# Performance work log

Hardware: AMD Instinct MI355X
Metric: run time of the kernel (lower is better)

The kernel has to match this reference:

```python
import jax, jax.numpy as jnp
import numpy as np


def setup_inputs() -> dict:
    key = jax.random.key(0)
    kx, kt = jax.random.split(key)
    b, n, d = 4, 4096, 1024
    x = jax.random.normal(kx, (b, n, d), dtype=jnp.float32)
    t = jax.random.normal(kt, (n, d), dtype=jnp.float32)
    return {"x": x, "t": t}


def reference(x, t):
    # y[b,i,d] = sum_{j<=i} t[i-j,d] * x[b,j,d]
    # Causal depthwise Toeplitz matvec == linear convolution truncated to n.
    # Computed via FFT along the sequence axis (zero-pad to 2n so the
    # circular convolution equals the linear one on the first n outputs).
    b, n, d = x.shape
    L = 2 * n
    xf = jnp.fft.rfft(x.astype(jnp.float32), n=L, axis=1)        # (b, L/2+1, d) complex
    tf = jnp.fft.rfft(t.astype(jnp.float32), n=L, axis=0)        # (L/2+1, d) complex
    y = jnp.fft.irfft(xf * tf[None], n=L, axis=1)[:, :n, :]      # (b, n, d)
    return y.astype(x.dtype)
```

## Files before the change

### kernel.cpp

```cpp
#include <hip/hip_runtime.h>

#define NT 512
#define SCL (1.0f / 8192.0f)
#define PI_F 3.14159265358979323846f

__device__ __forceinline__ int P(int i) { return i ^ ((i >> 5) & 31); }

__device__ __forceinline__ float2 cmul(float2 a, float2 b) {
  return make_float2(a.x * b.x - a.y * b.y, a.x * b.y + a.y * b.x);
}
__device__ __forceinline__ float2 csqr(float2 a) {
  return make_float2(a.x * a.x - a.y * a.y, 2.f * a.x * a.y);
}
__device__ __forceinline__ float2 cadd(float2 a, float2 b) { return make_float2(a.x + b.x, a.y + b.y); }
__device__ __forceinline__ float2 csub(float2 a, float2 b) { return make_float2(a.x - b.x, a.y - b.y); }
__device__ __forceinline__ float2 cmuli (float2 a) { return make_float2(-a.y,  a.x); }
__device__ __forceinline__ float2 cmulmi(float2 a) { return make_float2( a.y, -a.x); }

constexpr float RT2 = 0.70710678118654752440f;
constexpr float CQ1 = 0.92387953251128675613f;
constexpr float SQ1 = 0.38268343236508977173f;
constexpr float C8x[4] = {1.f,  RT2, 0.f, -RT2};
constexpr float C8y[4] = {0.f, -RT2, -1.f, -RT2};

template<bool UNIT>
__device__ __forceinline__ void r8_fwd(float2* e, float2 b) {
  float2 b2, b4;
  if (!UNIT) { b2 = csqr(b); b4 = csqr(b2); }
  #pragma unroll
  for (int j = 0; j < 4; ++j) {
    float2 u = e[j], v = e[j + 4];
    float2 d = csub(u, v);
    e[j] = cadd(u, v);
    float2 c8 = make_float2(C8x[j], C8y[j]);
    if (UNIT) e[j + 4] = (j == 0) ? d : cmul(d, c8);
    else      e[j + 4] = cmul(d, (j == 0) ? b : cmul(b, c8));
  }
  #pragma unroll
  for (int o = 0; o < 8; o += 4) {
    #pragma unroll
    for (int j = 0; j < 2; ++j) {
      float2 u = e[o + j], v = e[o + j + 2];
      float2 d = csub(u, v);
      e[o + j] = cadd(u, v);
      if (UNIT) e[o + j + 2] = (j == 0) ? d : cmulmi(d);
      else      e[o + j + 2] = cmul(d, (j == 0) ? b2 : cmulmi(b2));
    }
  }
  #pragma unroll
  for (int o = 0; o < 8; o += 2) {
    float2 u = e[o], v = e[o + 1];
    float2 d = csub(u, v);
    e[o] = cadd(u, v);
    e[o + 1] = UNIT ? d : cmul(d, b4);
  }
}

template<bool UNIT>
__device__ __forceinline__ void r8_inv(float2* e, float2 g) {
  float2 g2, g4;
  if (!UNIT) { g2 = csqr(g); g4 = csqr(g2); }
  #pragma unroll
  for (int o = 0; o < 8; o += 2) {
    float2 t = UNIT ? e[o + 1] : cmul(e[o + 1], g4);
    float2 u = e[o];
    e[o] = cadd(u, t); e[o + 1] = csub(u, t);
  }
  #pragma unroll
  for (int o = 0; o < 8; o += 4) {
    #pragma unroll
    for (int j = 0; j < 2; ++j) {
      float2 v = e[o + j + 2];
      float2 t;
      if (UNIT) t = (j == 0) ? v : cmuli(v);
      else      t = cmul(v, (j == 0) ? g2 : cmuli(g2));
      float2 u = e[o + j];
      e[o + j] = cadd(u, t); e[o + j + 2] = csub(u, t);
    }
  }
  #pragma unroll
  for (int j = 0; j < 4; ++j) {
    float2 v = e[j + 4];
    float2 t;
    float2 c8c = make_float2(C8x[j], -C8y[j]);
    if (UNIT) t = (j == 0) ? v : cmul(v, c8c);
    else      t = cmul(v, (j == 0) ? g : cmul(g, c8c));
    float2 u = e[j];
    e[j] = cadd(u, t); e[j + 4] = csub(u, t);
  }
}

__device__ __forceinline__ void trip8_fwd(float2* cb, int base, int G, float2 b) {
  #pragma unroll 1
  for (int g = 0; g < 2; ++g) {
    int bs = base + g * 4096;
    float2 e[8];
    #pragma unroll
    for (int j = 0; j < 8; ++j) e[j] = cb[P(bs + G * j)];
    r8_fwd<false>(e, b);
    #pragma unroll
    for (int j = 0; j < 8; ++j) cb[P(bs + G * j)] = e[j];
  }
}

__device__ __forceinline__ void trip8_inv(float2* cb, int base, int G, float2 g) {
  #pragma unroll 1
  for (int gg = 0; gg < 2; ++gg) {
    int bs = base + gg * 4096;
    float2 e[8];
    #pragma unroll
    for (int j = 0; j < 8; ++j) e[j] = cb[P(bs + G * j)];
    r8_inv<false>(e, g);
    #pragma unroll
    for (int j = 0; j < 8; ++j) cb[P(bs + G * j)] = e[j];
  }
}

__global__ __launch_bounds__(NT)
void fftconv(float* __restrict__ xT, const float* __restrict__ tT) {
  __shared__ float2 cb[8192];
  __shared__ float2 Th[8192];
  const int tid = threadIdx.x;
  const int d = blockIdx.x;

  const int baseA = tid;
  const int baseB = ((tid >> 6) << 9) + (tid & 63);
  const int baseC = ((tid >> 3) << 6) + (tid & 7);
  const int baseM = tid << 3;

  float s0, c0; __sincosf(-PI_F * (float)tid / 2048.f, &s0, &c0);
  const float2 bA = make_float2(c0, s0);
  float s1, c1; __sincosf(-PI_F * (float)(tid & 63) / 256.f, &s1, &c1);
  const float2 bB = make_float2(c1, s1);
  float s2, c2; __sincosf(-PI_F * (float)(tid & 7) / 32.f, &s2, &c2);
  const float2 bC = make_float2(c2, s2);
  float sw, cw; __sincosf(-PI_F * (float)tid / 4096.f, &sw, &cw);
  const float2 W0 = make_float2(cw, sw);
  const float2 ROT  = make_float2(CQ1, -SQ1);
  const float2 ROTc = make_float2(CQ1,  SQ1);

  {
    const float* tp = tT + (size_t)d * 4096;
    float2 w = W0;
    #pragma unroll
    for (int k = 0; k < 8; ++k) {
      int n = tid + NT * k;
      float tv = tp[n];
      cb[P(n)] = make_float2(tv, 0.f);
      cb[P(n + 4096)] = make_float2(tv * w.x, tv * w.y);
      w = cmul(w, ROT);
    }
  }
  __syncthreads();
  trip8_fwd(cb, baseA, 512, bA); __syncthreads();
  trip8_fwd(cb, baseB, 64,  bB); __syncthreads();
  trip8_fwd(cb, baseC, 8,   bC); __syncthreads();
  #pragma unroll 1
  for (int g = 0; g < 2; ++g) {
    int bs = baseM + g * 4096;
    float2 e[8];
    #pragma unroll
    for (int j = 0; j < 8; ++j) e[j] = cb[P(bs + j)];
    r8_fwd<true>(e, make_float2(1.f, 0.f));
    #pragma unroll
    for (int j = 0; j < 8; ++j) Th[P(bs + j)] = make_float2(e[j].x * SCL, e[j].y * SCL);
  }
  __syncthreads();

  #pragma unroll 1
  for (int pass = 0; pass < 2; ++pass) {
    float* r0 = xT + ((size_t)(2 * pass)     * 1024 + d) * 4096;
    float* r1 = xT + ((size_t)(2 * pass + 1) * 1024 + d) * 4096;
    {
      float2 w = W0;
      #pragma unroll
      for (int k = 0; k < 8; ++k) {
        int n = tid + NT * k;
        float2 v = make_float2(r0[n], r1[n]);
        cb[P(n)] = v;
        cb[P(n + 4096)] = cmul(v, w);
        w = cmul(w, ROT);
      }
    }
    __syncthreads();
    trip8_fwd(cb, baseA, 512, bA); __syncthreads();
    trip8_fwd(cb, baseB, 64,  bB); __syncthreads();
    trip8_fwd(cb, baseC, 8,   bC); __syncthreads();
    #pragma unroll 1
    for (int g = 0; g < 2; ++g) {
      int bs = baseM + g * 4096;
      float2 e[8];
      #pragma unroll
      for (int j = 0; j < 8; ++j) e[j] = cb[P(bs + j)];
      r8_fwd<true>(e, make_float2(1.f, 0.f));
      #pragma unroll
      for (int j = 0; j < 8; ++j) e[j] = cmul(e[j], Th[P(bs + j)]);
      r8_inv<true>(e, make_float2(1.f, 0.f));
      #pragma unroll
      for (int j = 0; j < 8; ++j) cb[P(bs + j)] = e[j];
    }
    __syncthreads();
    trip8_inv(cb, baseC, 8,   make_float2(bC.x, -bC.y)); __syncthreads();
    trip8_inv(cb, baseB, 64,  make_float2(bB.x, -bB.y)); __syncthreads();
    trip8_inv(cb, baseA, 512, make_float2(bA.x, -bA.y)); __syncthreads();
    {
      float2 w = make_float2(cw, -sw);
      #pragma unroll
      for (int k = 0; k < 8; ++k) {
        int n = tid + NT * k;
        float2 u = cb[P(n)];
        float2 v = cmul(cb[P(n + 4096)], w);
        r0[n] = u.x + v.x;
        r1[n] = u.y + v.y;
        w = cmul(w, ROTc);
      }
    }
    __syncthreads();
  }
}

__global__ __launch_bounds__(256)
void transpose64(const float* __restrict__ src, float* __restrict__ dst, int R, int C) {
  __shared__ float tile[64][65];
  int t  = threadIdx.x;
  int c4 = t & 15;
  int r  = t >> 4;
  size_t slab = (size_t)blockIdx.z * (size_t)R * (size_t)C;
  const float* s = src + slab;
  float* dd = dst + slab;
  int col0 = blockIdx.x * 64, row0 = blockIdx.y * 64;
  #pragma unroll
  for (int k = 0; k < 4; ++k) {
    int rr = r + 16 * k;
    const float4 v = *(const float4*)(s + (size_t)(row0 + rr) * C + col0 + 4 * c4);
    tile[rr][4 * c4 + 0] = v.x;
    tile[rr][4 * c4 + 1] = v.y;
    tile[rr][4 * c4 + 2] = v.z;
    tile[rr][4 * c4 + 3] = v.w;
  }
  __syncthreads();
  #pragma unroll
  for (int k = 0; k < 4; ++k) {
    int cc = r + 16 * k;
    float4 w;
    w.x = tile[4 * c4 + 0][cc];
    w.y = tile[4 * c4 + 1][cc];
    w.z = tile[4 * c4 + 2][cc];
    w.w = tile[4 * c4 + 3][cc];
    *(float4*)(dd + (size_t)(col0 + cc) * R + row0 + 4 * c4) = w;
  }
}

extern "C" void kernel_launch(void* const* d_in, const int* in_sizes, int n_in,
                              void* d_out, int out_size, void* d_ws, size_t ws_size,
                              hipStream_t stream) {
  const float* x = (const float*)d_in[0];
  const float* t = (const float*)d_in[1];
  float* out = (float*)d_out;
  float* ws  = (float*)d_ws;
  float* xT  = ws;
  float* tT  = ws + (size_t)4 * 1024 * 4096;

  transpose64<<<dim3(16, 64, 4), 256, 0, stream>>>(x, xT, 4096, 1024);
  transpose64<<<dim3(16, 64, 1), 256, 0, stream>>>(t, tT, 4096, 1024);

  fftconv<<<dim3(1024), NT, 0, stream>>>(xT, tT);

  transpose64<<<dim3(64, 16, 4), 256, 0, stream>>>(xT, out, 1024, 4096);
}
```

Measured before the change: 183.3 us.

## Precompute filter spectrum in separate kernel to halve fftconv shared memory

Moves the FFT of the Toeplitz filter t into its own kernel that writes the scaled spectrum to global memory, using the output buffer as scratch. The main fftconv kernel then loads the spectrum from global memory in the pointwise-multiply stage and keeps only one 64 KB shared buffer instead of two. The intent is to allow more blocks per CU and better latency hiding. The cost is an extra launch plus a write and reread of the spectrum through global memory, and the spectrum is now read once per pass rather than computed once per block.

```diff
diff --git a/kernel.cpp b/kernel.cpp
--- a/kernel.cpp
+++ b/kernel.cpp
@@ -117,9 +117,59 @@
 }
 
 __global__ __launch_bounds__(NT)
-void fftconv(float* __restrict__ xT, const float* __restrict__ tT) {
+void that8(const float* __restrict__ tT, float2* __restrict__ ThG) {
   __shared__ float2 cb[8192];
-  __shared__ float2 Th[8192];
+  const int tid = threadIdx.x;
+  const int d = blockIdx.x;
+
+  const int baseA = tid;
+  const int baseB = ((tid >> 6) << 9) + (tid & 63);
+  const int baseC = ((tid >> 3) << 6) + (tid & 7);
+  const int baseM = tid << 3;
+
+  float s0, c0; __sincosf(-PI_F * (float)tid / 2048.f, &s0, &c0);
+  const float2 bA = make_float2(c0, s0);
+  float s1, c1; __sincosf(-PI_F * (float)(tid & 63) / 256.f, &s1, &c1);
+  const float2 bB = make_float2(c1, s1);
+  float s2, c2; __sincosf(-PI_F * (float)(tid & 7) / 32.f, &s2, &c2);
+  const float2 bC = make_float2(c2, s2);
+  float sw, cw; __sincosf(-PI_F * (float)tid / 4096.f, &sw, &cw);
+  const float2 W0 = make_float2(cw, sw);
+  const float2 ROT = make_float2(CQ1, -SQ1);
+
+  {
+    const float* tp = tT + (size_t)d * 4096;
+    float2 w = W0;
+    #pragma unroll
+    for (int k = 0; k < 8; ++k) {
+      int n = tid + NT * k;
+      float tv = tp[n];
+      cb[P(n)] = make_float2(tv, 0.f);
+      cb[P(n + 4096)] = make_float2(tv * w.x, tv * w.y);
+      w = cmul(w, ROT);
+    }
+  }
+  __syncthreads();
+  trip8_fwd(cb, baseA, 512, bA); __syncthreads();
+  trip8_fwd(cb, baseB, 64,  bB); __syncthreads();
+  trip8_fwd(cb, baseC, 8,   bC); __syncthreads();
+  float2* thg = ThG + (size_t)d * 8192;
+  #pragma unroll 1
+  for (int g = 0; g < 2; ++g) {
+    int bs = baseM + g * 4096;
+    float2 e[8];
+    #pragma unroll
+    for (int j = 0; j < 8; ++j) e[j] = cb[P(bs + j)];
+    r8_fwd<true>(e, make_float2(1.f, 0.f));
+    #pragma unroll
+    for (int j = 0; j < 8; ++j)
+      thg[tid + 512 * j + 4096 * g] = make_float2(e[j].x * SCL, e[j].y * SCL);
+  }
+}
+
+__global__ __launch_bounds__(NT)
+void fftconv(float* __restrict__ xT, const float2* __restrict__ ThG) {
+  __shared__ float2 cb[8192];
   const int tid = threadIdx.x;
   const int d = blockIdx.x;
 
@@ -139,33 +189,7 @@
   const float2 ROT  = make_float2(CQ1, -SQ1);
   const float2 ROTc = make_float2(CQ1,  SQ1);
 
-  {
-    const float* tp = tT + (size_t)d * 4096;
-    float2 w = W0;
-    #pragma unroll
-    for (int k = 0; k < 8; ++k) {
-      int n = tid + NT * k;
-      float tv = tp[n];
-      cb[P(n)] = make_float2(tv, 0.f);
-      cb[P(n + 4096)] = make_float2(tv * w.x, tv * w.y);
-      w = cmul(w, ROT);
-    }
-  }
-  __syncthreads();
-  trip8_fwd(cb, baseA, 512, bA); __syncthreads();
-  trip8_fwd(cb, baseB, 64,  bB); __syncthreads();
-  trip8_fwd(cb, baseC, 8,   bC); __syncthreads();
-  #pragma unroll 1
-  for (int g = 0; g < 2; ++g) {
-    int bs = baseM + g * 4096;
-    float2 e[8];
-    #pragma unroll
-    for (int j = 0; j < 8; ++j) e[j] = cb[P(bs + j)];
-    r8_fwd<true>(e, make_float2(1.f, 0.f));
-    #pragma unroll
-    for (int j = 0; j < 8; ++j) Th[P(bs + j)] = make_float2(e[j].x * SCL, e[j].y * SCL);
-  }
-  __syncthreads();
+  const float2* thg = ThG + (size_t)d * 8192;
 
   #pragma unroll 1
   for (int pass = 0; pass < 2; ++pass) {
@@ -186,18 +210,33 @@
     trip8_fwd(cb, baseA, 512, bA); __syncthreads();
     trip8_fwd(cb, baseB, 64,  bB); __syncthreads();
     trip8_fwd(cb, baseC, 8,   bC); __syncthreads();
-    #pragma unroll 1
-    for (int g = 0; g < 2; ++g) {
-      int bs = baseM + g * 4096;
+    {
+      float2 th[8];
+      #pragma unroll
+      for (int j = 0; j < 8; ++j) th[j] = thg[tid + 512 * j];
       float2 e[8];
       #pragma unroll
-      for (int j = 0; j < 8; ++j) e[j] = cb[P(bs + j)];
+      for (int j = 0; j < 8; ++j) e[j] = cb[P(baseM + j)];
       r8_fwd<true>(e, make_float2(1.f, 0.f));
       #pragma unroll
-      for (int j = 0; j < 8; ++j) e[j] = cmul(e[j], Th[P(bs + j)]);
+      for (int j = 0; j < 8; ++j) e[j] = cmul(e[j], th[j]);
       r8_inv<true>(e, make_float2(1.f, 0.f));
       #pragma unroll
-      for (int j = 0; j < 8; ++j) cb[P(bs + j)] = e[j];
+      for (int j = 0; j < 8; ++j) cb[P(baseM + j)] = e[j];
+    }
+    {
+      float2 th[8];
+      #pragma unroll
+      for (int j = 0; j < 8; ++j) th[j] = thg[tid + 512 * j + 4096];
+      float2 e[8];
+      #pragma unroll
+      for (int j = 0; j < 8; ++j) e[j] = cb[P(baseM + 4096 + j)];
+      r8_fwd<true>(e, make_float2(1.f, 0.f));
+      #pragma unroll
+      for (int j = 0; j < 8; ++j) e[j] = cmul(e[j], th[j]);
+      r8_inv<true>(e, make_float2(1.f, 0.f));
+      #pragma unroll
+      for (int j = 0; j < 8; ++j) cb[P(baseM + 4096 + j)] = e[j];
     }
     __syncthreads();
     trip8_inv(cb, baseC, 8,   make_float2(bC.x, -bC.y)); __syncthreads();
@@ -260,11 +299,13 @@
   float* ws  = (float*)d_ws;
   float* xT  = ws;
   float* tT  = ws + (size_t)4 * 1024 * 4096;
+  float2* ThG = (float2*)d_out;
 
   transpose64<<<dim3(16, 64, 4), 256, 0, stream>>>(x, xT, 4096, 1024);
   transpose64<<<dim3(16, 64, 1), 256, 0, stream>>>(t, tT, 4096, 1024);
 
-  fftconv<<<dim3(1024), NT, 0, stream>>>(xT, tT);
+  that8<<<dim3(1024), NT, 0, stream>>>(tT, ThG);
+  fftconv<<<dim3(1024), NT, 0, stream>>>(xT, ThG);
 
   transpose64<<<dim3(64, 16, 4), 256, 0, stream>>>(xT, out, 1024, 4096);
 }
```

New measurement: 239.0 us. 30.4% more time.
